# Kernel optimization log

Hardware: AMD Instinct MI355X
Metric: run time of the kernel (lower is better)

The kernel has to match this reference:

```python
import jax, jax.numpy as jnp
import numpy as np

DIM = 128
DIM1 = 128
D_MODEL = DIM + DIM1          # 256
D_INNER = 2 * D_MODEL         # expand=2 -> 512
D_STATE = 16
D_CONV = 4
DT_RANK = (D_MODEL + 15) // 16  # ceil(d_model/16) = 16
B, H, W = 4, 64, 64


def layer_norm(x, g, b, eps=1e-5):
    mu = jnp.mean(x, axis=-1, keepdims=True)
    var = jnp.mean((x - mu) ** 2, axis=-1, keepdims=True)
    return (x - mu) * jax.lax.rsqrt(var + eps) * g + b


def setup_inputs() -> dict:
    key = jax.random.key(0)
    ks = jax.random.split(key, 16)
    s = lambda k, shape, scale: (jax.random.normal(k, shape, jnp.float32) * scale)
    inp = {
        "input": jax.random.normal(ks[0], (B, DIM, H, W), jnp.float32),
        "input2": jax.random.normal(ks[1], (B, DIM1, H, W), jnp.float32),
        # MambaB params
        "ln0_g": jnp.ones((D_MODEL,), jnp.float32),
        "ln0_b": jnp.zeros((D_MODEL,), jnp.float32),
        "outp_w": s(ks[2], (D_MODEL, DIM), 1.0 / np.sqrt(D_MODEL)),
        "outp_b": jnp.zeros((DIM,), jnp.float32),
        # Mamba params
        "in_proj_w": s(ks[3], (D_MODEL, 2 * D_INNER), 1.0 / np.sqrt(D_MODEL)),
        "conv_w": s(ks[4], (D_INNER, D_CONV), 1.0 / np.sqrt(D_CONV)),
        "conv_b": jnp.zeros((D_INNER,), jnp.float32),
        "x_proj_w": s(ks[5], (D_INNER, DT_RANK + 2 * D_STATE), 1.0 / np.sqrt(D_INNER)),
        "dt_proj_w": s(ks[6], (DT_RANK, D_INNER), 1.0 / np.sqrt(DT_RANK)),
        "dt_proj_b": s(ks[7], (D_INNER,), 0.1),
        "A_log": jnp.log(jnp.tile(jnp.arange(1.0, D_STATE + 1.0, dtype=jnp.float32), (D_INNER, 1))),
        "D_param": jnp.ones((D_INNER,), jnp.float32),
        "mamba_out_w": s(ks[8], (D_INNER, D_MODEL), 1.0 / np.sqrt(D_INNER)),
    }
    return inp


def mamba(x, in_proj_w, conv_w, conv_b, x_proj_w, dt_proj_w, dt_proj_b, A_log, D_param, mamba_out_w):
    b, L, _ = x.shape
    xz = x @ in_proj_w                       # [b, L, 2*di]
    xs, z = jnp.split(xz, 2, axis=-1)
    # causal depthwise conv over sequence
    xt = xs.transpose(0, 2, 1)               # [b, di, L]
    conv = jax.lax.conv_general_dilated(
        xt, conv_w[:, None, :], window_strides=(1,),
        padding=[(D_CONV - 1, 0)], feature_group_count=D_INNER)
    xs = jax.nn.silu(conv + conv_b[None, :, None]).transpose(0, 2, 1)  # [b, L, di]
    x_dbl = xs @ x_proj_w                    # [b, L, dt_rank + 2*n]
    dt = x_dbl[..., :DT_RANK]
    Bm = x_dbl[..., DT_RANK:DT_RANK + D_STATE]
    Cm = x_dbl[..., DT_RANK + D_STATE:]
    delta = jax.nn.softplus(dt @ dt_proj_w + dt_proj_b)  # [b, L, di]
    A = -jnp.exp(A_log)                      # [di, n]

    def step(h, t):
        d_t, B_t, C_t, x_t = t               # [b,di],[b,n],[b,n],[b,di]
        dA = jnp.exp(d_t[:, :, None] * A)    # [b, di, n]
        h = h * dA + (d_t * x_t)[:, :, None] * B_t[:, None, :]
        y = jnp.einsum('bdn,bn->bd', h, C_t)
        return h, y

    h0 = jnp.zeros((b, D_INNER, D_STATE), x.dtype)
    _, ys = jax.lax.scan(step, h0, (delta.transpose(1, 0, 2), Bm.transpose(1, 0, 2),
                                    Cm.transpose(1, 0, 2), xs.transpose(1, 0, 2)))
    y = ys.transpose(1, 0, 2) + xs * D_param
    y = y * jax.nn.silu(z)
    return y @ mamba_out_w                   # [b, L, d_model]


def reference(input, input2, ln0_g, ln0_b, outp_w, outp_b, in_proj_w, conv_w, conv_b,
              x_proj_w, dt_proj_w, dt_proj_b, A_log, D_param, mamba_out_w):
    b, c, h, w = input.shape
    x = jnp.concatenate((input, input2), axis=1)            # [b, d_model, h, w]
    x = x.reshape(b, D_MODEL, h * w).transpose(0, 2, 1)     # [b, hw, d_model]
    x = layer_norm(x, ln0_g, ln0_b)
    out = mamba(x, in_proj_w, conv_w, conv_b, x_proj_w, dt_proj_w, dt_proj_b,
                A_log, D_param, mamba_out_w)
    out = out @ outp_w + outp_b                             # [b, hw, dim]
    return out.transpose(0, 2, 1).reshape(b, c, h, w)
```

## Files before the change

### kernel.cpp

```cpp
#include <hip/hip_runtime.h>
#include <hip/hip_bf16.h>
#include <math.h>

#define LSEQ 4096
#define NR   16384
#define NB   4
#define CHUNK 32
#define NCH  128

typedef short bf16x8 __attribute__((ext_vector_type(8)));
typedef float f32x4  __attribute__((ext_vector_type(4)));
typedef float f32x2  __attribute__((ext_vector_type(2)));

typedef __attribute__((address_space(1))) const void gvoid_t;
typedef __attribute__((address_space(3))) void svoid_t;

__device__ __forceinline__ void gld_lds16(void* lds, const void* g) {
    __builtin_amdgcn_global_load_lds((gvoid_t*)g, (svoid_t*)lds, 16, 0, 0);
}

__device__ __forceinline__ unsigned short to_bf16(float f) {
    union { float f; unsigned u; } x; x.f = f;
    unsigned r = (x.u + 0x7fff + ((x.u >> 16) & 1)) >> 16;
    return (unsigned short)r;
}
__device__ __forceinline__ float bf2f(unsigned short u) {
    union { unsigned u; float f; } x; x.u = ((unsigned)u) << 16;
    return x.f;
}
__device__ __forceinline__ float softplus_f(float x) {
    return x > 20.f ? x : __logf(1.f + __expf(x));
}
__device__ __forceinline__ float silu_f(float x) {
    return x / (1.f + __expf(-x));
}

__device__ __forceinline__ void pow_chain16_pk(float r, f32x2* a2) {
    float r2 = r * r;
    float r4 = r2 * r2;
    float r8 = r4 * r4;
    f32x2 v01 = { r, r2 };
    a2[0] = v01;
    a2[1] = v01 * r2;
    a2[2] = v01 * r4;
    a2[3] = a2[1] * r4;
    a2[4] = v01 * r8;
    a2[5] = a2[1] * r8;
    a2[6] = a2[2] * r8;
    a2[7] = a2[3] * r8;
}

__device__ __forceinline__ bool pow_ok16(const float* An) {
    bool ok = true;
    #pragma unroll
    for (int n = 1; n < 16; ++n) {
        float ref = (float)(n + 1) * An[0];
        ok = ok && (fabsf(An[n] - ref) <= 1e-4f * fabsf(An[n]) + 1e-30f);
    }
    return ok;
}

__global__ __launch_bounds__(256) void front_kernel(const float* __restrict__ in1,
                                                    const float* __restrict__ in2,
                                                    const float* __restrict__ g,
                                                    const float* __restrict__ beta,
                                                    const float* __restrict__ Wm,
                                                    const float* __restrict__ Wo,
                                                    const float* __restrict__ Wxp,
                                                    const float* __restrict__ A_log,
                                                    const float* __restrict__ W,
                                                    unsigned short* __restrict__ Abf,
                                                    unsigned short* __restrict__ WcT,
                                                    unsigned short* __restrict__ Wxpt,
                                                    float* __restrict__ anegp,
                                                    unsigned short* __restrict__ Wt) {
    __shared__ float tile[256][33];
    int blk = blockIdx.x;
    int tid = threadIdx.x;
    if (blk < 512) {
        __shared__ float s1[8][32], s2[8][32];
        __shared__ float smu[32], srs[32];
        int b  = blk >> 7;
        int t0 = (blk & 127) * 32;
        #pragma unroll
        for (int p = 0; p < 8; ++p) {
            int c = p * 32 + (tid >> 3);
            int toff = (tid & 7) * 4;
            const float* src = (c < 128) ? &in1[((size_t)(b * 128 + c)) * LSEQ + t0 + toff]
                                         : &in2[((size_t)(b * 128 + (c - 128))) * LSEQ + t0 + toff];
            float4 v = *(const float4*)src;
            tile[c][toff] = v.x; tile[c][toff+1] = v.y;
            tile[c][toff+2] = v.z; tile[c][toff+3] = v.w;
        }
        __syncthreads();
        {
            int t = tid & 31, gg = tid >> 5;
            float a1 = 0.f, a2 = 0.f;
            #pragma unroll
            for (int i = 0; i < 32; ++i) {
                float v = tile[gg * 32 + i][t];
                a1 += v; a2 += v * v;
            }
            s1[gg][t] = a1; s2[gg][t] = a2;
        }
        __syncthreads();
        if (tid < 32) {
            float a1 = 0.f, a2 = 0.f;
            #pragma unroll
            for (int gg = 0; gg < 8; ++gg) { a1 += s1[gg][tid]; a2 += s2[gg][tid]; }
            float m = a1 * (1.f / 256.f);
            float var = a2 * (1.f / 256.f) - m * m;
            smu[tid] = m;
            srs[tid] = rsqrtf(var + 1e-5f);
        }
        __syncthreads();
        int c = tid;
        float gc = g[c], bc = beta[c];
        #pragma unroll 4
        for (int t = 0; t < 32; ++t) {
            float v = (tile[c][t] - smu[t]) * srs[t] * gc + bc;
            Abf[((size_t)((b << 12) + t0 + t)) * 256 + c] = to_bf16(v);
        }
    } else if (blk < 768) {
        int gid = (blk - 512) * 256 + tid;
        int row = gid >> 7, col = gid & 127;
        float acc = 0.f;
        #pragma unroll 8
        for (int k = 0; k < 256; ++k) acc += Wm[row * 256 + k] * Wo[k * 128 + col];
        WcT[(size_t)col * 512 + row] = to_bf16(acc);
    } else if (blk < 864) {
        int gid = (blk - 768) * 256 + tid;
        int n = gid >> 9, k = gid & 511;
        Wxpt[gid] = to_bf16(Wxp[(size_t)k * 48 + n]);
    } else if (blk < 896) {
        int gid = (blk - 864) * 256 + tid;
        anegp[gid] = -__expf(A_log[gid]);
    } else {
        float* tf = &tile[0][0];
        int local = blk - 896;
        int k0 = (local & 3) * 64;
        int n0 = (local >> 2) * 64;
        int a = tid & 63, q = tid >> 6;
        #pragma unroll
        for (int i = 0; i < 16; ++i) {
            int k = q * 16 + i;
            tf[k * 65 + a] = W[(size_t)(k0 + k) * 1024 + n0 + a];
        }
        __syncthreads();
        #pragma unroll
        for (int i = 0; i < 16; ++i) {
            int n = q * 16 + i;
            Wt[(size_t)(n0 + n) * 256 + k0 + a] = to_bf16(tf[a * 65 + n]);
        }
    }
}

__global__ __launch_bounds__(256) void gemm1_mfma(const unsigned short* __restrict__ Abf,
                                                  const unsigned short* __restrict__ Wt,
                                                  unsigned short* __restrict__ xh,
                                                  unsigned short* __restrict__ zs) {
    __shared__ __align__(16) short Asl[128][32];
    __shared__ __align__(16) short Bsl[128][32];
    int tid = threadIdx.x;
    int wv = tid >> 6, ln = tid & 63;
    int m0 = blockIdx.x * 128;
    int n0 = blockIdx.y * 128;
    int mw = (wv & 1) * 64, nw = (wv >> 1) * 64;

    f32x4 acc[4][4];
    #pragma unroll
    for (int i = 0; i < 4; ++i)
        #pragma unroll
        for (int j = 0; j < 4; ++j) acc[i][j] = (f32x4)(0.f);

    int srow  = ln >> 2;
    int skoff = (ln & 3) * 8;

    for (int k0 = 0; k0 < 256; k0 += 32) {
        #pragma unroll
        for (int i = 0; i < 2; ++i) {
            int j = wv * 2 + i;
            int row = j * 16 + srow;
            gld_lds16(&Asl[j * 16][0], &Abf[(size_t)(m0 + row) * 256 + k0 + skoff]);
            gld_lds16(&Bsl[j * 16][0], &Wt [(size_t)(n0 + row) * 256 + k0 + skoff]);
        }
        __syncthreads();
        bf16x8 af[4], bff[4];
        int fm = ln & 15, fk = (ln >> 4) * 8;
        #pragma unroll
        for (int i = 0; i < 4; ++i) {
            af[i]  = *(const bf16x8*)&Asl[mw + i * 16 + fm][fk];
            bff[i] = *(const bf16x8*)&Bsl[nw + i * 16 + fm][fk];
        }
        #pragma unroll
        for (int i = 0; i < 4; ++i)
            #pragma unroll
            for (int j = 0; j < 4; ++j)
                acc[i][j] = __builtin_amdgcn_mfma_f32_16x16x32_bf16(af[i], bff[j], acc[i][j], 0, 0, 0);
        __syncthreads();
    }
    int ccol = ln & 15, crow = (ln >> 4) * 4;
    bool zhalf = (n0 >= 512);
    #pragma unroll
    for (int i = 0; i < 4; ++i) {
        #pragma unroll
        for (int j = 0; j < 4; ++j) {
            int n = n0 + nw + j * 16 + ccol;
            #pragma unroll
            for (int r = 0; r < 4; ++r) {
                int m = m0 + mw + i * 16 + crow + r;
                float v = acc[i][j][r];
                if (zhalf) zs[(size_t)m * 512 + (n - 512)] = to_bf16(silu_f(v));
                else       xh[(size_t)m * 512 + n]         = to_bf16(v);
            }
        }
    }
}

__global__ __launch_bounds__(512, 4) void mid_kernel(const unsigned short* __restrict__ xh,
                                                     const float* __restrict__ cw,
                                                     const float* __restrict__ cb,
                                                     const unsigned short* __restrict__ Wxpt,
                                                     const float* __restrict__ Wdt,
                                                     const float* __restrict__ dtb,
                                                     const float* __restrict__ anegp,
                                                     unsigned* __restrict__ dxp,
                                                     float* __restrict__ xdbl,
                                                     float* __restrict__ Sarr,
                                                     float* __restrict__ Harr) {
    __shared__ __align__(16) unsigned short xcs[CHUNK][520];
    __shared__ __align__(16) float xds[CHUNK][48];
    int tid = threadIdx.x;
    int chunk = blockIdx.x & (NCH - 1);
    int b     = blockIdx.x >> 7;
    int d = tid;
    int rbase = (b << 12) + chunk * CHUNK;

    float4 w4 = *(const float4*)&cw[d * 4];
    float cbd = cb[d];
    float An[16];
    #pragma unroll
    for (int n = 0; n < 16; n += 4) {
        float4 v = *(const float4*)&anegp[d * 16 + n];
        An[n] = v.x; An[n+1] = v.y; An[n+2] = v.z; An[n+3] = v.w;
    }
    f32x2 wdt2[8];
    #pragma unroll
    for (int q = 0; q < 8; ++q) {
        wdt2[q].x = Wdt[(2 * q) * 512 + d];
        wdt2[q].y = Wdt[(2 * q + 1) * 512 + d];
    }
    float bd = dtb[d];

    float x0 = 0.f, x1 = 0.f, x2 = 0.f;
    if (chunk > 0) {
        x0 = bf2f(xh[(size_t)(rbase - 3) * 512 + d]);
        x1 = bf2f(xh[(size_t)(rbase - 2) * 512 + d]);
        x2 = bf2f(xh[(size_t)(rbase - 1) * 512 + d]);
    }
    #pragma unroll
    for (int t = 0; t < CHUNK; ++t) {
        float x3 = bf2f(xh[(size_t)(rbase + t) * 512 + d]);
        float a = x0 * w4.x + x1 * w4.y + x2 * w4.z + x3 * w4.w + cbd;
        xcs[t][d] = to_bf16(silu_f(a));
        x0 = x1; x1 = x2; x2 = x3;
    }
    __syncthreads();

    {
        int wv = tid >> 6, ln = tid & 63;
        if (wv < 6) {
            int mt = (wv >= 3) ? 16 : 0;
            int wr = (wv >= 3) ? wv - 3 : wv;
            int nt = wr * 16;
            int fm = ln & 15, fk = (ln >> 4) * 8;
            f32x4 acc = (f32x4)(0.f);
            #pragma unroll 4
            for (int k0 = 0; k0 < 512; k0 += 32) {
                bf16x8 af  = *(const bf16x8*)&xcs[mt + fm][k0 + fk];
                bf16x8 bf_ = *(const bf16x8*)&Wxpt[(size_t)(nt + fm) * 512 + k0 + fk];
                acc = __builtin_amdgcn_mfma_f32_16x16x32_bf16(af, bf_, acc, 0, 0, 0);
            }
            int ccol = ln & 15, crow = (ln >> 4) * 4;
            #pragma unroll
            for (int r = 0; r < 4; ++r)
                xds[mt + crow + r][nt + ccol] = acc[r];
        }
    }
    __syncthreads();

    #pragma unroll
    for (int i = 0; i < 2; ++i) {
        int idx = tid + i * 512;
        int t = idx >> 5, n = idx & 31;
        xdbl[(size_t)(rbase + t) * 32 + n] = xds[t][16 + n];
    }

    bool pm = pow_ok16(An);
    f32x2 h2[8];
    #pragma unroll
    for (int n = 0; n < 8; ++n) h2[n] = (f32x2)(0.f);
    float S = 0.f;
    const f32x2* xds2 = (const f32x2*)&xds[0][0];
    if (pm) {
        float An0 = An[0];
        #pragma unroll 4
        for (int t = 0; t < CHUNK; ++t) {
            f32x2 acc2 = { bd, 0.f };
            #pragma unroll
            for (int q = 0; q < 8; ++q)
                acc2 = acc2 + xds2[t * 24 + q] * wdt2[q];
            float a = acc2.x + acc2.y;
            unsigned short dbf = to_bf16(softplus_f(a));
            unsigned short xbf = xcs[t][d];
            float dv = bf2f(dbf), xv = bf2f(xbf);
            dxp[(size_t)(rbase + t) * 512 + d] = (unsigned)dbf | ((unsigned)xbf << 16);
            float dx = dv * xv;
            S += dv;
            f32x2 a2[8];
            pow_chain16_pk(__expf(dv * An0), a2);
            #pragma unroll
            for (int g = 0; g < 8; ++g)
                h2[g] = h2[g] * a2[g] + dx * xds2[t * 24 + 8 + g];
        }
    } else {
        #pragma unroll 2
        for (int t = 0; t < CHUNK; ++t) {
            f32x2 acc2 = { bd, 0.f };
            #pragma unroll
            for (int q = 0; q < 8; ++q)
                acc2 = acc2 + xds2[t * 24 + q] * wdt2[q];
            float a = acc2.x + acc2.y;
            unsigned short dbf = to_bf16(softplus_f(a));
            unsigned short xbf = xcs[t][d];
            float dv = bf2f(dbf), xv = bf2f(xbf);
            dxp[(size_t)(rbase + t) * 512 + d] = (unsigned)dbf | ((unsigned)xbf << 16);
            float dx = dv * xv;
            S += dv;
            #pragma unroll
            for (int g = 0; g < 8; ++g) {
                f32x2 e = { __expf(dv * An[2*g]), __expf(dv * An[2*g+1]) };
                h2[g] = h2[g] * e + dx * xds2[t * 24 + 8 + g];
            }
        }
    }
    Sarr[(size_t)chunk * 2048 + b * 512 + d] = S;
    size_t gbase = ((size_t)(b * 512 + d)) * 16;
    size_t coff  = (size_t)chunk * 32768;
    #pragma unroll
    for (int n = 0; n < 4; ++n) {
        *(float4*)&Harr[coff + gbase + n * 4] =
            make_float4(h2[2*n].x, h2[2*n].y, h2[2*n+1].x, h2[2*n+1].y);
    }
}

__global__ __launch_bounds__(256) void scan_pass2(const float* __restrict__ Sarr,
                                                  const float* __restrict__ anegp,
                                                  float* __restrict__ Harr) {
    int gid = blockIdx.x * 256 + threadIdx.x;
    float An = anegp[gid & 8191];
    int sidx = gid >> 4;
    float carry = 0.f;
    #pragma unroll 8
    for (int c = 0; c < NCH; ++c) {
        float S  = Sarr[(size_t)c * 2048 + sidx];
        size_t off = (size_t)c * 32768 + gid;
        float he = Harr[off];
        Harr[off] = carry;
        carry = he + __expf(S * An) * carry;
    }
}

__global__ __launch_bounds__(256) void scan_pass3(const unsigned* __restrict__ dxp,
                                                  const unsigned short* __restrict__ zs,
                                                  const float* __restrict__ xdbl,
                                                  const float* __restrict__ anegp,
                                                  const float* __restrict__ Dp,
                                                  const float* __restrict__ Hin,
                                                  unsigned short* __restrict__ yf16) {
    __shared__ __align__(16) float4 sB4[CHUNK][4];
    __shared__ __align__(16) float4 sC4[CHUNK][4];
    int tid = threadIdx.x;
    int chunk = blockIdx.x & (NCH - 1);
    int half  = (blockIdx.x >> 7) & 1;
    int b     = blockIdx.x >> 8;
    int d = half * 256 + tid;
    int rbase = (b << 12) + chunk * CHUNK;
    unsigned pwv[CHUNK];
    #pragma unroll
    for (int t = 0; t < CHUNK; ++t)
        pwv[t] = dxp[(size_t)(rbase + t) * 512 + d];
    {
        float* sBf = (float*)sB4;
        float* sCf = (float*)sC4;
        #pragma unroll
        for (int i = 0; i < 2; ++i) {
            int e = tid + i * 256;
            int t = e >> 4, n = e & 15;
            sBf[t * 16 + n] = xdbl[(size_t)(rbase + t) * 32 + n];
            sCf[t * 16 + n] = xdbl[(size_t)(rbase + t) * 32 + 16 + n];
        }
    }
    float An[16];
    #pragma unroll
    for (int n = 0; n < 16; n += 4) {
        float4 v = *(const float4*)&anegp[d * 16 + n];
        An[n] = v.x; An[n+1] = v.y; An[n+2] = v.z; An[n+3] = v.w;
    }
    bool pm = pow_ok16(An);
    float Dv = Dp[d];
    __syncthreads();
    size_t gbase = ((size_t)(b * 512 + d)) * 16;
    size_t coff  = (size_t)chunk * 32768;
    f32x2 h2[8];
    #pragma unroll
    for (int n = 0; n < 4; ++n) {
        float4 v = *(const float4*)&Hin[coff + gbase + n * 4];
        h2[2*n].x = v.x; h2[2*n].y = v.y; h2[2*n+1].x = v.z; h2[2*n+1].y = v.w;
    }
    const f32x2* sB2 = (const f32x2*)&sB4[0][0];
    const f32x2* sC2 = (const f32x2*)&sC4[0][0];
    if (pm) {
        float An0 = An[0];
        #pragma unroll 8
        for (int t = 0; t < CHUNK; ++t) {
            unsigned pw = pwv[t];
            float dv = bf2f((unsigned short)(pw & 0xffffu));
            float xv = bf2f((unsigned short)(pw >> 16));
            float zv = bf2f(zs[(size_t)(rbase + t) * 512 + d]);
            float dx = dv * xv;
            f32x2 a2[8];
            pow_chain16_pk(__expf(dv * An0), a2);
            f32x2 y2 = (f32x2)(0.f);
            #pragma unroll
            for (int g = 0; g < 8; ++g) {
                h2[g] = h2[g] * a2[g] + dx * sB2[t * 8 + g];
                y2 = y2 + h2[g] * sC2[t * 8 + g];
            }
            float y = y2.x + y2.y + xv * Dv;
            y *= zv;
            yf16[(size_t)(rbase + t) * 512 + d] = to_bf16(y);
        }
    } else {
        #pragma unroll 4
        for (int t = 0; t < CHUNK; ++t) {
            unsigned pw = pwv[t];
            float dv = bf2f((unsigned short)(pw & 0xffffu));
            float xv = bf2f((unsigned short)(pw >> 16));
            float zv = bf2f(zs[(size_t)(rbase + t) * 512 + d]);
            float dx = dv * xv;
            f32x2 y2 = (f32x2)(0.f);
            #pragma unroll
            for (int g = 0; g < 8; ++g) {
                f32x2 e = { __expf(dv * An[2*g]), __expf(dv * An[2*g+1]) };
                h2[g] = h2[g] * e + dx * sB2[t * 8 + g];
                y2 = y2 + h2[g] * sC2[t * 8 + g];
            }
            float y = y2.x + y2.y + xv * Dv;
            y *= zv;
            yf16[(size_t)(rbase + t) * 512 + d] = to_bf16(y);
        }
    }
}

__global__ __launch_bounds__(256) void gemm_out_mfma(const unsigned short* __restrict__ WcT,
                                                     const unsigned short* __restrict__ yf16,
                                                     const float* __restrict__ bo,
                                                     float* __restrict__ out) {
    __shared__ __align__(16) short Asl[128][32];
    __shared__ __align__(16) short Bsl[64][32];
    int tid = threadIdx.x;
    int wv = tid >> 6, ln = tid & 63;
    int n0 = blockIdx.x * 64;
    int mw = (wv & 1) * 64, nw = (wv >> 1) * 32;

    f32x4 acc[4][2];
    #pragma unroll
    for (int i = 0; i < 4; ++i)
        #pragma unroll
        for (int j = 0; j < 2; ++j) acc[i][j] = (f32x4)(0.f);

    int srow  = ln >> 2;
    int skoff = (ln & 3) * 8;

    for (int k0 = 0; k0 < 512; k0 += 32) {
        #pragma unroll
        for (int i = 0; i < 2; ++i) {
            int j = wv * 2 + i;
            int row = j * 16 + srow;
            gld_lds16(&Asl[j * 16][0], &WcT[(size_t)row * 512 + k0 + skoff]);
        }
        {
            int row = wv * 16 + srow;
            gld_lds16(&Bsl[wv * 16][0], &yf16[(size_t)(n0 + row) * 512 + k0 + skoff]);
        }
        __syncthreads();
        bf16x8 af[4], bff[2];
        int fm = ln & 15, fk = (ln >> 4) * 8;
        #pragma unroll
        for (int i = 0; i < 4; ++i) af[i]  = *(const bf16x8*)&Asl[mw + i * 16 + fm][fk];
        #pragma unroll
        for (int j = 0; j < 2; ++j) bff[j] = *(const bf16x8*)&Bsl[nw + j * 16 + fm][fk];
        #pragma unroll
        for (int i = 0; i < 4; ++i)
            #pragma unroll
            for (int j = 0; j < 2; ++j)
                acc[i][j] = __builtin_amdgcn_mfma_f32_16x16x32_bf16(af[i], bff[j], acc[i][j], 0, 0, 0);
        __syncthreads();
    }
    int ccol = ln & 15, crow = (ln >> 4) * 4;
    int b = n0 >> 12, tb = n0 & 4095;
    #pragma unroll
    for (int i = 0; i < 4; ++i) {
        #pragma unroll
        for (int r = 0; r < 4; ++r) {
            int c = mw + i * 16 + crow + r;
            float bias = bo[c];
            #pragma unroll
            for (int j = 0; j < 2; ++j) {
                int t = tb + nw + j * 16 + ccol;
                out[((size_t)(b * 128 + c)) * LSEQ + t] = acc[i][j][r] + bias;
            }
        }
    }
}

extern "C" void kernel_launch(void* const* d_in, const int* in_sizes, int n_in,
                              void* d_out, int out_size, void* d_ws, size_t ws_size,
                              hipStream_t stream) {
    (void)in_sizes; (void)n_in; (void)out_size; (void)ws_size;
    const float* input    = (const float*)d_in[0];
    const float* input2   = (const float*)d_in[1];
    const float* ln_g     = (const float*)d_in[2];
    const float* ln_b     = (const float*)d_in[3];
    const float* outp_w   = (const float*)d_in[4];
    const float* outp_b   = (const float*)d_in[5];
    const float* in_proj  = (const float*)d_in[6];
    const float* conv_w   = (const float*)d_in[7];
    const float* conv_b   = (const float*)d_in[8];
    const float* x_proj   = (const float*)d_in[9];
    const float* dt_w     = (const float*)d_in[10];
    const float* dt_b     = (const float*)d_in[11];
    const float* A_log    = (const float*)d_in[12];
    const float* D_param  = (const float*)d_in[13];
    const float* mout_w   = (const float*)d_in[14];
    float* out = (float*)d_out;

    char* ws = (char*)d_ws;
    unsigned short* xh    = (unsigned short*)ws;                    ws += (size_t)NR * 512 * 2;
    unsigned short* zsbuf = (unsigned short*)ws;                    ws += (size_t)NR * 512 * 2;
    unsigned short* yf16  = (unsigned short*)ws;                    ws += (size_t)NR * 512 * 2;
    unsigned*       dxp   = (unsigned*)ws;                          ws += (size_t)NR * 512 * 4;
    unsigned short* Abf   = (unsigned short*)ws;                    ws += (size_t)NR * 256 * 2;
    unsigned short* Wt    = (unsigned short*)ws;                    ws += (size_t)1024 * 256 * 2;
    unsigned short* WcT   = (unsigned short*)ws;                    ws += (size_t)128 * 512 * 2;
    unsigned short* Wxpt  = (unsigned short*)ws;                    ws += (size_t)48 * 512 * 2;
    float* anegp = (float*)ws;                                      ws += (size_t)512 * 16 * 4;
    float* xdbl = (float*)ws;                                       ws += (size_t)NR * 32 * 4;
    float* Sarr = (float*)ws;                                       ws += (size_t)NCH * 2048 * 4;
    float* Harr = (float*)ws;                                       ws += (size_t)NCH * 32768 * 4;

    front_kernel<<<960, 256, 0, stream>>>(input, input2, ln_g, ln_b, mout_w, outp_w,
                                          x_proj, A_log, in_proj,
                                          Abf, WcT, Wxpt, anegp, Wt);
    gemm1_mfma<<<dim3(128, 8), 256, 0, stream>>>(Abf, Wt, xh, zsbuf);
    mid_kernel<<<NB * NCH, 512, 0, stream>>>(xh, conv_w, conv_b, Wxpt, dt_w, dt_b,
                                             anegp, dxp, xdbl, Sarr, Harr);
    scan_pass2<<<128, 256, 0, stream>>>(Sarr, anegp, Harr);
    scan_pass3<<<NB * NCH * 2, 256, 0, stream>>>(dxp, zsbuf, xdbl, anegp, D_param,
                                                 Harr, yf16);
    gemm_out_mfma<<<NR / 64, 256, 0, stream>>>(WcT, yf16, outp_b, out);
}
```

Before: 207.4 us.

## Fuse scan pass3 with output projection GEMM via LDS-staged y tile

Merges the final scan pass and the output projection GEMM into one kernel. Each 512-thread block covers all 512 channels of a 32-step chunk, writes y as bf16 into shared memory, then 8 waves run MFMA against the combined weight read straight from global memory to produce 128 output channels. This drops the y round trip through global memory and one kernel launch. The cost is 512 blocks of 512 threads instead of 1024 blocks of 256, more LDS per block, and un-staged weight loads in the GEMM phase.

```diff
diff --git a/kernel.cpp b/kernel.cpp
--- a/kernel.cpp
+++ b/kernel.cpp
@@ -371,20 +371,22 @@
     }
 }
 
-__global__ __launch_bounds__(256) void scan_pass3(const unsigned* __restrict__ dxp,
-                                                  const unsigned short* __restrict__ zs,
-                                                  const float* __restrict__ xdbl,
-                                                  const float* __restrict__ anegp,
-                                                  const float* __restrict__ Dp,
-                                                  const float* __restrict__ Hin,
-                                                  unsigned short* __restrict__ yf16) {
+__global__ __launch_bounds__(512, 4) void scan_pass3_out(const unsigned* __restrict__ dxp,
+                                                         const unsigned short* __restrict__ zs,
+                                                         const float* __restrict__ xdbl,
+                                                         const float* __restrict__ anegp,
+                                                         const float* __restrict__ Dp,
+                                                         const float* __restrict__ Hin,
+                                                         const unsigned short* __restrict__ WcT,
+                                                         const float* __restrict__ bo,
+                                                         float* __restrict__ out) {
+    __shared__ __align__(16) unsigned short yl[CHUNK][520];
     __shared__ __align__(16) float4 sB4[CHUNK][4];
     __shared__ __align__(16) float4 sC4[CHUNK][4];
     int tid = threadIdx.x;
     int chunk = blockIdx.x & (NCH - 1);
-    int half  = (blockIdx.x >> 7) & 1;
-    int b     = blockIdx.x >> 8;
-    int d = half * 256 + tid;
+    int b     = blockIdx.x >> 7;
+    int d = tid;
     int rbase = (b << 12) + chunk * CHUNK;
     unsigned pwv[CHUNK];
     #pragma unroll
@@ -393,13 +395,9 @@
     {
         float* sBf = (float*)sB4;
         float* sCf = (float*)sC4;
-        #pragma unroll
-        for (int i = 0; i < 2; ++i) {
-            int e = tid + i * 256;
-            int t = e >> 4, n = e & 15;
-            sBf[t * 16 + n] = xdbl[(size_t)(rbase + t) * 32 + n];
-            sCf[t * 16 + n] = xdbl[(size_t)(rbase + t) * 32 + 16 + n];
-        }
+        int t = tid >> 4, n = tid & 15;
+        sBf[t * 16 + n] = xdbl[(size_t)(rbase + t) * 32 + n];
+        sCf[t * 16 + n] = xdbl[(size_t)(rbase + t) * 32 + 16 + n];
     }
     float An[16];
     #pragma unroll
@@ -439,7 +437,7 @@
             }
             float y = y2.x + y2.y + xv * Dv;
             y *= zv;
-            yf16[(size_t)(rbase + t) * 512 + d] = to_bf16(y);
+            yl[t][d] = to_bf16(y);
         }
     } else {
         #pragma unroll 4
@@ -458,69 +456,32 @@
             }
             float y = y2.x + y2.y + xv * Dv;
             y *= zv;
-            yf16[(size_t)(rbase + t) * 512 + d] = to_bf16(y);
-        }
-    }
-}
-
-__global__ __launch_bounds__(256) void gemm_out_mfma(const unsigned short* __restrict__ WcT,
-                                                     const unsigned short* __restrict__ yf16,
-                                                     const float* __restrict__ bo,
-                                                     float* __restrict__ out) {
-    __shared__ __align__(16) short Asl[128][32];
-    __shared__ __align__(16) short Bsl[64][32];
-    int tid = threadIdx.x;
-    int wv = tid >> 6, ln = tid & 63;
-    int n0 = blockIdx.x * 64;
-    int mw = (wv & 1) * 64, nw = (wv >> 1) * 32;
-
-    f32x4 acc[4][2];
-    #pragma unroll
-    for (int i = 0; i < 4; ++i)
-        #pragma unroll
-        for (int j = 0; j < 2; ++j) acc[i][j] = (f32x4)(0.f);
-
-    int srow  = ln >> 2;
-    int skoff = (ln & 3) * 8;
-
-    for (int k0 = 0; k0 < 512; k0 += 32) {
-        #pragma unroll
-        for (int i = 0; i < 2; ++i) {
-            int j = wv * 2 + i;
-            int row = j * 16 + srow;
-            gld_lds16(&Asl[j * 16][0], &WcT[(size_t)row * 512 + k0 + skoff]);
-        }
-        {
-            int row = wv * 16 + srow;
-            gld_lds16(&Bsl[wv * 16][0], &yf16[(size_t)(n0 + row) * 512 + k0 + skoff]);
-        }
-        __syncthreads();
-        bf16x8 af[4], bff[2];
+            yl[t][d] = to_bf16(y);
+        }
+    }
+    __syncthreads();
+
+    {
+        int wv = tid >> 6, ln = tid & 63;
         int fm = ln & 15, fk = (ln >> 4) * 8;
-        #pragma unroll
-        for (int i = 0; i < 4; ++i) af[i]  = *(const bf16x8*)&Asl[mw + i * 16 + fm][fk];
-        #pragma unroll
-        for (int j = 0; j < 2; ++j) bff[j] = *(const bf16x8*)&Bsl[nw + j * 16 + fm][fk];
-        #pragma unroll
-        for (int i = 0; i < 4; ++i)
-            #pragma unroll
-            for (int j = 0; j < 2; ++j)
-                acc[i][j] = __builtin_amdgcn_mfma_f32_16x16x32_bf16(af[i], bff[j], acc[i][j], 0, 0, 0);
-        __syncthreads();
-    }
-    int ccol = ln & 15, crow = (ln >> 4) * 4;
-    int b = n0 >> 12, tb = n0 & 4095;
-    #pragma unroll
-    for (int i = 0; i < 4; ++i) {
+        f32x4 acc0 = (f32x4)(0.f), acc1 = (f32x4)(0.f);
+        const unsigned short* wrow = &WcT[(size_t)(wv * 16 + fm) * 512];
+        #pragma unroll 4
+        for (int k0 = 0; k0 < 512; k0 += 32) {
+            bf16x8 af = *(const bf16x8*)&wrow[k0 + fk];
+            bf16x8 b0 = *(const bf16x8*)&yl[fm][k0 + fk];
+            bf16x8 b1 = *(const bf16x8*)&yl[16 + fm][k0 + fk];
+            acc0 = __builtin_amdgcn_mfma_f32_16x16x32_bf16(af, b0, acc0, 0, 0, 0);
+            acc1 = __builtin_amdgcn_mfma_f32_16x16x32_bf16(af, b1, acc1, 0, 0, 0);
+        }
+        int ccol = ln & 15, crow = (ln >> 4) * 4;
         #pragma unroll
         for (int r = 0; r < 4; ++r) {
-            int c = mw + i * 16 + crow + r;
+            int c = wv * 16 + crow + r;
             float bias = bo[c];
-            #pragma unroll
-            for (int j = 0; j < 2; ++j) {
-                int t = tb + nw + j * 16 + ccol;
-                out[((size_t)(b * 128 + c)) * LSEQ + t] = acc[i][j][r] + bias;
-            }
+            size_t obase = ((size_t)(b * 128 + c)) * LSEQ + chunk * CHUNK;
+            out[obase + ccol]      = acc0[r] + bias;
+            out[obase + 16 + ccol] = acc1[r] + bias;
         }
     }
 }
@@ -549,7 +510,6 @@
     char* ws = (char*)d_ws;
     unsigned short* xh    = (unsigned short*)ws;                    ws += (size_t)NR * 512 * 2;
     unsigned short* zsbuf = (unsigned short*)ws;                    ws += (size_t)NR * 512 * 2;
-    unsigned short* yf16  = (unsigned short*)ws;                    ws += (size_t)NR * 512 * 2;
     unsigned*       dxp   = (unsigned*)ws;                          ws += (size_t)NR * 512 * 4;
     unsigned short* Abf   = (unsigned short*)ws;                    ws += (size_t)NR * 256 * 2;
     unsigned short* Wt    = (unsigned short*)ws;                    ws += (size_t)1024 * 256 * 2;
@@ -567,7 +527,6 @@
     mid_kernel<<<NB * NCH, 512, 0, stream>>>(xh, conv_w, conv_b, Wxpt, dt_w, dt_b,
                                              anegp, dxp, xdbl, Sarr, Harr);
     scan_pass2<<<128, 256, 0, stream>>>(Sarr, anegp, Harr);
-    scan_pass3<<<NB * NCH * 2, 256, 0, stream>>>(dxp, zsbuf, xdbl, anegp, D_param,
-                                                 Harr, yf16);
-    gemm_out_mfma<<<NR / 64, 256, 0, stream>>>(WcT, yf16, outp_b, out);
-}
+    scan_pass3_out<<<NB * NCH, 512, 0, stream>>>(dxp, zsbuf, xdbl, anegp, D_param,
+                                                 Harr, WcT, outp_b, out);
+}
```

Result: no change. 204.9 us (-1.2%).
